# Optimization experiments

Measured on AMD Instinct MI355X. Metric: run time of the kernel, lower is better.

The kernel has to match this reference:

```python
import jax, jax.numpy as jnp
import numpy as np

B, TQ, TK = 64, 1, 2048
QD, KD, U, H = 512, 512, 1024, 8
D = U // H  # per-head dim = 128


def setup_inputs() -> dict:
    key0 = jax.random.key(0)
    k0, k1, k2, k3, k4 = jax.random.split(key0, 5)
    query = jax.random.normal(k0, (B, TQ, QD), jnp.float32)
    key = jax.random.normal(k1, (B, TK, KD), jnp.float32)
    # 1x1 Conv1d == Linear: weight [out_ch, in_ch], bias [out_ch]
    Wq = jax.random.normal(k2, (U, QD), jnp.float32) / np.sqrt(QD).astype(np.float32)
    bq = jnp.zeros((U,), jnp.float32)
    Wk = jax.random.normal(k3, (U, KD), jnp.float32) / np.sqrt(KD).astype(np.float32)
    bk = jnp.zeros((U,), jnp.float32)
    # v is generated with torch.randn every forward in the original (unlearned);
    # here it is a fixed random vector of size D (per-head units).
    v = jax.random.normal(k4, (D,), jnp.float32)
    return {"query": query, "key": key, "Wq": Wq, "bq": bq, "Wk": Wk, "bk": bk, "v": v}


def reference(query, key, Wq, bq, Wk, bk, v):
    # 1x1 conv projections (channels-last linear)
    q = jnp.einsum('btq,uq->btu', query, Wq) + bq          # [B,TQ,U]
    k = jnp.einsum('btk,uk->btu', key, Wk) + bk            # [B,TK,U]
    # split heads: torch.stack(torch.split(x, D, dim=2), dim=1) -> [B,H,T,D]
    qs = q.reshape(B, TQ, H, D).transpose(0, 2, 1, 3)      # [B,H,TQ,D]
    ks = k.reshape(B, TK, H, D).transpose(0, 2, 1, 3)      # [B,H,TK,D]
    # weight-normalized random projection vector (b is zeros, folded away)
    g = np.float32(1.0) / np.sqrt(D).astype(np.float32)
    normed_v = g * v * jax.lax.rsqrt(jnp.sum(v * v))       # [D]
    # additive score: sum_d normed_v * tanh(ks + qs)  (qs broadcasts over TK)
    add = jnp.einsum('d,bhtd->bht', normed_v, jnp.tanh(ks + qs))  # [B,H,TK]
    # F.softmax without dim on a 4D tensor -> legacy dim=1 (heads axis)
    weights = jax.nn.softmax(add[:, :, None, :], axis=1)   # [B,H,TQ,TK]
    # value = unprojected key, shared across heads
    context = jnp.einsum('bhqt,btd->bhqd', weights, key)   # [B,H,TQ,KD]
    # view(B, TQ, -1): valid because TQ == 1
    return context.reshape(B, TQ, H * KD)
```

## Files before the change

kernel.cpp:

```cpp
#include <hip/hip_runtime.h>

#define B_   64
#define TK_  2048
#define KD_  512
#define U_   1024
#define H_   8
#define D_   128
#define MT   64
#define APAD 8
#define ASTR (KD_ + APAD)
#define NTILE (TK_ / MT)
#define GRID (B_ * NTILE)

typedef float f32x4 __attribute__((ext_vector_type(4)));
typedef short short8 __attribute__((ext_vector_type(8)));

__device__ __forceinline__ short f2bf(float f) {
    unsigned u = __float_as_uint(f);
    u += 0x7fffu + ((u >> 16) & 1u);
    return (short)(u >> 16);
}
__device__ __forceinline__ float bf2f(short s) {
    return __uint_as_float(((unsigned)(unsigned short)s) << 16);
}
__device__ __forceinline__ float tanh_fast(float x) {
    float e = __builtin_amdgcn_exp2f(x * 2.885390081777927f);
    return 1.0f - 2.0f * __builtin_amdgcn_rcpf(1.0f + e);
}

__global__ void nv_kernel(const float* __restrict__ v, float* __restrict__ wsNV) {
    __shared__ float red[D_];
    int tid = threadIdx.x;
    float x = v[tid];
    red[tid] = x * x;
    __syncthreads();
    if (tid == 0) {
        float s = 0.f;
        for (int i = 0; i < D_; ++i) s += red[i];
        red[0] = rsqrtf(s) * 0.08838834764831845f;
    }
    __syncthreads();
    wsNV[tid] = x * red[0];
}

__global__ void q_kernel(const float* __restrict__ query, const float* __restrict__ Wq,
                         const float* __restrict__ bq, const float* __restrict__ bk,
                         float* __restrict__ wsQ) {
    __shared__ float qrow[KD_];
    int b = blockIdx.x, ug = blockIdx.y, tid = threadIdx.x;
    if (tid < 128) ((float4*)qrow)[tid] = ((const float4*)(query + (size_t)b * KD_))[tid];
    __syncthreads();
    int u = ug * 256 + tid;
    const float4* wq = (const float4*)(Wq + (size_t)u * KD_);
    const float4* q4 = (const float4*)qrow;
    float acc = 0.f;
#pragma unroll 8
    for (int i = 0; i < KD_ / 4; ++i) {
        float4 a = q4[i], w = wq[i];
        acc += a.x * w.x + a.y * w.y + a.z * w.z + a.w * w.w;
    }
    wsQ[(size_t)b * U_ + u] = acc + bq[u] + bk[u];
}

__global__ void swz_kernel(const float* __restrict__ Wk, short* __restrict__ wsB) {
    int g = blockIdx.x * 256 + threadIdx.x;
    int slot = g >> 6, l = g & 63;
    int ublk = slot >> 4, ks = slot & 15;
    int u = ublk * 16 + (l & 15);
    int k0 = ks * 32 + ((l >> 4) << 3);
    const float* src = Wk + (size_t)u * KD_ + k0;
    short8 o;
#pragma unroll
    for (int j = 0; j < 8; ++j) o[j] = f2bf(src[j]);
    *(short8*)(wsB + (size_t)g * 8) = o;
}

template <bool ATOMIC>
__global__ __launch_bounds__(256, 2) void attn_kernel(
    const float* __restrict__ key, const short* __restrict__ wsB,
    const float* __restrict__ wsQ, const float* __restrict__ wsNV,
    float* __restrict__ outp)
{
    __shared__ short As[MT * ASTR];
    __shared__ float S[MT][H_];
    __shared__ float Wt[MT][H_];

    int bx = blockIdx.x;
    int b = bx & 63, tt = bx >> 6;
    int tid = threadIdx.x;

    const float4* src = (const float4*)(key + ((size_t)b * TK_ + (size_t)tt * MT) * KD_);
#pragma unroll 8
    for (int j = 0; j < 32; ++j) {
        int i = tid + j * 256;
        float4 v = src[i];
        int t = i >> 7, c4 = (i & 127) << 2;
        short4 h4;
        h4.x = f2bf(v.x); h4.y = f2bf(v.y); h4.z = f2bf(v.z); h4.w = f2bf(v.w);
        *(short4*)&As[t * ASTR + c4] = h4;
    }
    __syncthreads();

    int w = tid >> 6, l = tid & 63;
    int l15 = l & 15, lq = l >> 4;
    const short8* bp = (const short8*)wsB;

    for (int c = 0; c < 2; ++c) {
        int ub = c * 512 + w * 128;
        int ub16 = ub >> 4;
        int bidx = ub16 * 1024 + l;

        f32x4 acc[4][8] = {};

        short8 bc[8];
#pragma unroll
        for (int nf = 0; nf < 8; ++nf) bc[nf] = bp[bidx + nf * 1024];

#pragma unroll 1
        for (int ks = 0; ks < 16; ++ks) {
            short8 bn[8];
            if (ks < 15) {
#pragma unroll
                for (int nf = 0; nf < 8; ++nf) bn[nf] = bp[bidx + nf * 1024 + (ks + 1) * 64];
            }
            short8 a[4];
#pragma unroll
            for (int mf = 0; mf < 4; ++mf)
                a[mf] = *(const short8*)&As[(mf * 16 + l15) * ASTR + ks * 32 + (lq << 3)];
#pragma unroll
            for (int mf = 0; mf < 4; ++mf)
#pragma unroll
                for (int nf = 0; nf < 8; ++nf)
                    acc[mf][nf] = __builtin_amdgcn_mfma_f32_16x16x32_bf16(a[mf], bc[nf], acc[mf][nf], 0, 0, 0);
            if (ks < 15) {
#pragma unroll
                for (int nf = 0; nf < 8; ++nf) bc[nf] = bn[nf];
            }
        }

        float qv[8], nv[8];
#pragma unroll
        for (int nf = 0; nf < 8; ++nf) {
            int d = nf * 16 + l15;
            qv[nf] = wsQ[(size_t)b * U_ + ub + d];
            nv[nf] = wsNV[d];
        }
        int h = ub >> 7;
#pragma unroll
        for (int mf = 0; mf < 4; ++mf)
#pragma unroll
            for (int r = 0; r < 4; ++r) {
                float p = 0.f;
#pragma unroll
                for (int nf = 0; nf < 8; ++nf)
                    p += nv[nf] * tanh_fast(acc[mf][nf][r] + qv[nf]);
                p += __shfl_xor(p, 1);
                p += __shfl_xor(p, 2);
                p += __shfl_xor(p, 4);
                p += __shfl_xor(p, 8);
                if (l15 == 0) S[mf * 16 + lq * 4 + r][h] = p;
            }
    }
    __syncthreads();

    if (tid < MT) {
        float sv[H_];
        float mx = -1e30f;
#pragma unroll
        for (int h = 0; h < H_; ++h) { sv[h] = S[tid][h]; mx = fmaxf(mx, sv[h]); }
        float sum = 0.f;
#pragma unroll
        for (int h = 0; h < H_; ++h) {
            sv[h] = __builtin_amdgcn_exp2f((sv[h] - mx) * 1.4426950408889634f);
            sum += sv[h];
        }
        float inv = __builtin_amdgcn_rcpf(sum);
#pragma unroll
        for (int h = 0; h < H_; ++h) Wt[tid][h] = sv[h] * inv;
    }
    __syncthreads();

    int dg = (tid & 127) << 2;
    int hb = (tid >> 7) << 2;
    float cacc[4][4] = {};
    for (int t = 0; t < MT; ++t) {
        short4 kk = *(const short4*)&As[t * ASTR + dg];
        float k0 = bf2f(kk.x), k1 = bf2f(kk.y), k2 = bf2f(kk.z), k3 = bf2f(kk.w);
#pragma unroll
        for (int j = 0; j < 4; ++j) {
            float wt = Wt[t][hb + j];
            cacc[j][0] += wt * k0; cacc[j][1] += wt * k1;
            cacc[j][2] += wt * k2; cacc[j][3] += wt * k3;
        }
    }
    if (ATOMIC) {
        float* ob = outp + (size_t)b * (H_ * KD_);
#pragma unroll
        for (int j = 0; j < 4; ++j)
#pragma unroll
            for (int d = 0; d < 4; ++d)
                atomicAdd(&ob[(hb + j) * KD_ + dg + d], cacc[j][d]);
    } else {
        float* pb = outp + (size_t)bx * (H_ * KD_);
#pragma unroll
        for (int j = 0; j < 4; ++j)
            *(f32x4*)&pb[(hb + j) * KD_ + dg] = *(f32x4*)&cacc[j][0];
    }
}

__global__ void reduce_kernel(const float* __restrict__ partial, float* __restrict__ out) {
    int o = blockIdx.x * 256 + threadIdx.x;
    int b = o >> 10;
    int u4 = o & 1023;
    const f32x4* p4 = (const f32x4*)partial;
    f32x4 s = {0.f, 0.f, 0.f, 0.f};
#pragma unroll 8
    for (int tt = 0; tt < NTILE; ++tt)
        s += p4[((size_t)(tt * 64 + b)) * 1024 + u4];
    ((f32x4*)out)[o] = s;
}

extern "C" void kernel_launch(void* const* d_in, const int* in_sizes, int n_in,
                              void* d_out, int out_size, void* d_ws, size_t ws_size,
                              hipStream_t stream) {
    const float* query = (const float*)d_in[0];
    const float* key   = (const float*)d_in[1];
    const float* Wq    = (const float*)d_in[2];
    const float* bq    = (const float*)d_in[3];
    const float* Wk    = (const float*)d_in[4];
    const float* bk    = (const float*)d_in[5];
    const float* v     = (const float*)d_in[6];
    float* out = (float*)d_out;

    char* ws = (char*)d_ws;
    float* wsNV = (float*)ws;
    float* wsQ  = (float*)(ws + 4096);
    short* wsB  = (short*)(ws + 524288);
    float* wsP  = (float*)(ws + 2 * 1024 * 1024);

    size_t need = 2 * 1024 * 1024 + (size_t)GRID * (H_ * KD_) * sizeof(float);

    nv_kernel<<<1, 128, 0, stream>>>(v, wsNV);
    q_kernel<<<dim3(64, 4), 256, 0, stream>>>(query, Wq, bq, bk, wsQ);
    swz_kernel<<<256, 256, 0, stream>>>(Wk, wsB);

    if (ws_size >= need) {
        attn_kernel<false><<<GRID, 256, 0, stream>>>(key, wsB, wsQ, wsNV, wsP);
        reduce_kernel<<<256, 256, 0, stream>>>(wsP, out);
    } else {
        hipMemsetAsync(d_out, 0, (size_t)out_size * sizeof(float), stream);
        attn_kernel<true><<<GRID, 256, 0, stream>>>(key, wsB, wsQ, wsNV, out);
    }
}
```

Before: 526.6 us.

## Re-layout swizzled Wk and software-pipeline B fragment prefetch across head chunks

Changes the swizzled Wk layout so each k-step's fragments for all u-blocks are contiguous, then restructures the MFMA loop into a double-buffered ping-pong that prefetches B fragments two steps ahead. The first B loads are issued before the key tile is staged into LDS, and the second chunk's loads start while the first chunk finishes. It also raises MFMA wave priority with s_setprio, hoists the q/nv loads, and vectorizes the softmax and context LDS reads. The aim is to hide global-load latency for the weight fragments, at the cost of more live registers under the 2-blocks-per-CU launch bound.

```diff
diff --git a/kernel.cpp b/kernel.cpp
--- a/kernel.cpp
+++ b/kernel.cpp
@@ -72,8 +72,54 @@
     short8 o;
 #pragma unroll
     for (int j = 0; j < 8; ++j) o[j] = f2bf(src[j]);
-    *(short8*)(wsB + (size_t)g * 8) = o;
-}
+    int oslot = ks * 64 + ublk;
+    *(short8*)(wsB + ((size_t)oslot * 64 + l) * 8) = o;
+}
+
+
+#define LOAD_A(a_, ksv)                                                               \
+    _Pragma("unroll")                                                                 \
+    for (int mf = 0; mf < 4; ++mf)                                                    \
+        a_[mf] = *(const short8*)&As[(mf * 16 + l15) * ASTR + (ksv) * 32 + (lq << 3)];
+
+#define MFMA32(a_, buf)                                                               \
+    __builtin_amdgcn_s_setprio(1);                                                    \
+    _Pragma("unroll")                                                                 \
+    for (int mf = 0; mf < 4; ++mf)                                                    \
+        _Pragma("unroll")                                                             \
+        for (int nf = 0; nf < 8; ++nf)                                                \
+            acc[mf][nf] = __builtin_amdgcn_mfma_f32_16x16x32_bf16(a_[mf], buf[nf],    \
+                                                                  acc[mf][nf], 0, 0, 0); \
+    __builtin_amdgcn_s_setprio(0);
+
+#define PREF_B(buf, pidx)                                                             \
+    _Pragma("unroll")                                                                 \
+    for (int nf = 0; nf < 8; ++nf) buf[nf] = bp[(pidx) + nf * 64];
+
+#define GSTEP(ksv, buf, pidx) { short8 a_[4]; LOAD_A(a_, ksv); MFMA32(a_, buf); PREF_B(buf, pidx); }
+#define GSTEP_NP(ksv, buf)    { short8 a_[4]; LOAD_A(a_, ksv); MFMA32(a_, buf); }
+
+#define ZERO_ACC                                                                      \
+    _Pragma("unroll")                                                                 \
+    for (int mf = 0; mf < 4; ++mf)                                                    \
+        _Pragma("unroll")                                                             \
+        for (int nf = 0; nf < 8; ++nf) acc[mf][nf] = (f32x4){0.f, 0.f, 0.f, 0.f};
+
+#define SCORE_EPI(qv, hh)                                                             \
+    _Pragma("unroll")                                                                 \
+    for (int mf = 0; mf < 4; ++mf)                                                    \
+        _Pragma("unroll")                                                             \
+        for (int r = 0; r < 4; ++r) {                                                 \
+            float p = 0.f;                                                            \
+            _Pragma("unroll")                                                         \
+            for (int nf = 0; nf < 8; ++nf)                                            \
+                p += nv8[nf] * tanh_fast(acc[mf][nf][r] + qv[nf]);                    \
+            p += __shfl_xor(p, 1);                                                    \
+            p += __shfl_xor(p, 2);                                                    \
+            p += __shfl_xor(p, 4);                                                    \
+            p += __shfl_xor(p, 8);                                                    \
+            if (l15 == 0) S[mf * 16 + lq * 4 + r][hh] = p;                            \
+        }
 
 template <bool ATOMIC>
 __global__ __launch_bounds__(256, 2) void attn_kernel(
@@ -88,6 +134,25 @@
     int bx = blockIdx.x;
     int b = bx & 63, tt = bx >> 6;
     int tid = threadIdx.x;
+    int w = tid >> 6, l = tid & 63;
+    int l15 = l & 15, lq = l >> 4;
+    const short8* bp = (const short8*)wsB;
+
+    int ub0 = w * 128, ub1 = 512 + w * 128;
+    int bidx0 = (ub0 >> 4) * 64 + l;
+    int bidx1 = (ub1 >> 4) * 64 + l;
+
+    short8 bbA[8], bbB[8];
+    PREF_B(bbA, bidx0);
+    PREF_B(bbB, bidx0 + 4096);
+
+    float nv8[8], qv0[8], qv1[8];
+#pragma unroll
+    for (int nf = 0; nf < 8; ++nf) {
+        int d = nf * 16 + l15;
+        nv8[nf] = wsNV[d];
+        qv0[nf] = wsQ[(size_t)b * U_ + ub0 + d];
+    }
 
     const float4* src = (const float4*)(key + ((size_t)b * TK_ + (size_t)tt * MT) * KD_);
 #pragma unroll 8
@@ -101,96 +166,68 @@
     }
     __syncthreads();
 
-    int w = tid >> 6, l = tid & 63;
-    int l15 = l & 15, lq = l >> 4;
-    const short8* bp = (const short8*)wsB;
-
-    for (int c = 0; c < 2; ++c) {
-        int ub = c * 512 + w * 128;
-        int ub16 = ub >> 4;
-        int bidx = ub16 * 1024 + l;
-
-        f32x4 acc[4][8] = {};
-
-        short8 bc[8];
-#pragma unroll
-        for (int nf = 0; nf < 8; ++nf) bc[nf] = bp[bidx + nf * 1024];
-
+    f32x4 acc[4][8];
+
+    ZERO_ACC;
 #pragma unroll 1
-        for (int ks = 0; ks < 16; ++ks) {
-            short8 bn[8];
-            if (ks < 15) {
-#pragma unroll
-                for (int nf = 0; nf < 8; ++nf) bn[nf] = bp[bidx + nf * 1024 + (ks + 1) * 64];
-            }
-            short8 a[4];
-#pragma unroll
-            for (int mf = 0; mf < 4; ++mf)
-                a[mf] = *(const short8*)&As[(mf * 16 + l15) * ASTR + ks * 32 + (lq << 3)];
-#pragma unroll
-            for (int mf = 0; mf < 4; ++mf)
-#pragma unroll
-                for (int nf = 0; nf < 8; ++nf)
-                    acc[mf][nf] = __builtin_amdgcn_mfma_f32_16x16x32_bf16(a[mf], bc[nf], acc[mf][nf], 0, 0, 0);
-            if (ks < 15) {
-#pragma unroll
-                for (int nf = 0; nf < 8; ++nf) bc[nf] = bn[nf];
-            }
-        }
-
-        float qv[8], nv[8];
-#pragma unroll
-        for (int nf = 0; nf < 8; ++nf) {
-            int d = nf * 16 + l15;
-            qv[nf] = wsQ[(size_t)b * U_ + ub + d];
-            nv[nf] = wsNV[d];
-        }
-        int h = ub >> 7;
-#pragma unroll
-        for (int mf = 0; mf < 4; ++mf)
-#pragma unroll
-            for (int r = 0; r < 4; ++r) {
-                float p = 0.f;
-#pragma unroll
-                for (int nf = 0; nf < 8; ++nf)
-                    p += nv[nf] * tanh_fast(acc[mf][nf][r] + qv[nf]);
-                p += __shfl_xor(p, 1);
-                p += __shfl_xor(p, 2);
-                p += __shfl_xor(p, 4);
-                p += __shfl_xor(p, 8);
-                if (l15 == 0) S[mf * 16 + lq * 4 + r][h] = p;
-            }
-    }
+    for (int ks = 0; ks < 14; ks += 2) {
+        GSTEP(ks,     bbA, bidx0 + (ks + 2) * 4096);
+        GSTEP(ks + 1, bbB, bidx0 + (ks + 3) * 4096);
+    }
+    GSTEP(14, bbA, bidx1);
+#pragma unroll
+    for (int nf = 0; nf < 8; ++nf) qv1[nf] = wsQ[(size_t)b * U_ + ub1 + nf * 16 + l15];
+    GSTEP(15, bbB, bidx1 + 4096);
+    SCORE_EPI(qv0, w);
+
+    ZERO_ACC;
+#pragma unroll 1
+    for (int ks = 0; ks < 14; ks += 2) {
+        GSTEP(ks,     bbA, bidx1 + (ks + 2) * 4096);
+        GSTEP(ks + 1, bbB, bidx1 + (ks + 3) * 4096);
+    }
+    GSTEP_NP(14, bbA);
+    GSTEP_NP(15, bbB);
+    SCORE_EPI(qv1, 4 + w);
     __syncthreads();
 
     if (tid < MT) {
-        float sv[H_];
-        float mx = -1e30f;
-#pragma unroll
-        for (int h = 0; h < H_; ++h) { sv[h] = S[tid][h]; mx = fmaxf(mx, sv[h]); }
+        f32x4 s0 = *(const f32x4*)&S[tid][0];
+        f32x4 s1 = *(const f32x4*)&S[tid][4];
+        float mx = fmaxf(fmaxf(fmaxf(s0[0], s0[1]), fmaxf(s0[2], s0[3])),
+                         fmaxf(fmaxf(s1[0], s1[1]), fmaxf(s1[2], s1[3])));
+        f32x4 e0, e1;
         float sum = 0.f;
 #pragma unroll
-        for (int h = 0; h < H_; ++h) {
-            sv[h] = __builtin_amdgcn_exp2f((sv[h] - mx) * 1.4426950408889634f);
-            sum += sv[h];
+        for (int h = 0; h < 4; ++h) {
+            e0[h] = __builtin_amdgcn_exp2f((s0[h] - mx) * 1.4426950408889634f);
+            sum += e0[h];
+        }
+#pragma unroll
+        for (int h = 0; h < 4; ++h) {
+            e1[h] = __builtin_amdgcn_exp2f((s1[h] - mx) * 1.4426950408889634f);
+            sum += e1[h];
         }
         float inv = __builtin_amdgcn_rcpf(sum);
 #pragma unroll
-        for (int h = 0; h < H_; ++h) Wt[tid][h] = sv[h] * inv;
+        for (int h = 0; h < 4; ++h) { e0[h] *= inv; e1[h] *= inv; }
+        *(f32x4*)&Wt[tid][0] = e0;
+        *(f32x4*)&Wt[tid][4] = e1;
     }
     __syncthreads();
 
     int dg = (tid & 127) << 2;
     int hb = (tid >> 7) << 2;
     float cacc[4][4] = {};
+#pragma unroll 4
     for (int t = 0; t < MT; ++t) {
         short4 kk = *(const short4*)&As[t * ASTR + dg];
+        f32x4 wt4 = *(const f32x4*)&Wt[t][hb];
         float k0 = bf2f(kk.x), k1 = bf2f(kk.y), k2 = bf2f(kk.z), k3 = bf2f(kk.w);
 #pragma unroll
         for (int j = 0; j < 4; ++j) {
-            float wt = Wt[t][hb + j];
-            cacc[j][0] += wt * k0; cacc[j][1] += wt * k1;
-            cacc[j][2] += wt * k2; cacc[j][3] += wt * k3;
+            cacc[j][0] += wt4[j] * k0; cacc[j][1] += wt4[j] * k1;
+            cacc[j][2] += wt4[j] * k2; cacc[j][3] += wt4[j] * k3;
         }
     }
     if (ATOMIC) {
```

Result: faster. 510.1 us (-3.1%).
